# Optimization experiments

Hardware: AMD Instinct MI355X
Metric: run time of the kernel (lower is better)

Reference implementation:

```python
import jax, jax.numpy as jnp
import numpy as np


def setup_inputs() -> dict:
    key = jax.random.key(0)
    T, B, D, R = 1024, 32, 1024, 256
    ks = jax.random.split(key, 6)
    scale = 1.0 / np.sqrt(D)
    x = jax.random.normal(ks[0], (T, B, D), dtype=jnp.float32)
    h0 = jnp.zeros((B, D), dtype=jnp.float32)
    W_alpha = jax.random.normal(ks[1], (D, D), dtype=jnp.float32) * scale
    b_alpha = jnp.full((D,), 2.0, dtype=jnp.float32)  # init_alpha_bias
    U = jax.random.normal(ks[2], (D, R), dtype=jnp.float32) * (0.5 / np.sqrt(R))
    V = jax.random.normal(ks[3], (R, D), dtype=jnp.float32) * (0.5 * scale)
    W_x = jax.random.normal(ks[4], (D, D), dtype=jnp.float32) * scale
    b = jnp.zeros((D,), dtype=jnp.float32)
    return {"x": x, "h0": h0, "W_alpha": W_alpha, "b_alpha": b_alpha,
            "U": U, "V": V, "W_x": W_x, "b": b}


def reference(x, h0, W_alpha, b_alpha, U, V, W_x, b):
    # Precompute input projections for all timesteps (as in the torch fallback)
    alpha_x_all = jnp.einsum('tbd,ed->tbe', x, W_alpha) + b_alpha  # [T,B,D]
    Wx_all = jnp.einsum('tbd,ed->tbe', x, W_x) + b                 # [T,B,D]

    def step(h_prev, inp):
        ax, wx = inp
        alpha = jax.nn.sigmoid(ax)                       # retain gate
        v = jnp.tanh((h_prev @ V.T) @ U.T + wx)          # low-rank h mixing
        h_new = alpha * h_prev + (1.0 - alpha) * v
        out = h_new * jax.nn.silu(h_new)
        return h_new, (h_new, out)

    _, (h_seq, output) = jax.lax.scan(step, h0, (alpha_x_all, Wx_all))
    h = jnp.concatenate([h0[None], h_seq], axis=0)       # [T+1,B,D]
    return output, h
```

## Files before the change

### kernel.cpp

```cpp
#include <hip/hip_runtime.h>

typedef _Float16 f16;
typedef f16 f16x2 __attribute__((ext_vector_type(2)));
typedef f16 f16x8 __attribute__((ext_vector_type(8)));
typedef float f32x4 __attribute__((ext_vector_type(4)));

#define TT 1024
#define BB 32
#define DD 1024
#define RR 256

__device__ __forceinline__ float dot2f(f16x2 a, f16x2 b, float c) {
#if __has_builtin(__builtin_amdgcn_fdot2)
    return __builtin_amdgcn_fdot2(a, b, c, false);
#else
    return c + (float)a[0] * (float)b[0] + (float)a[1] * (float)b[1];
#endif
}

__device__ __forceinline__ float sigm_f(float x) { return 1.0f / (1.0f + __expf(-x)); }
__device__ __forceinline__ float tanh_f(float x) { return 1.0f - 2.0f / (1.0f + __expf(2.0f * x)); }

__global__ __launch_bounds__(256)
void fused_pregemm(const float* __restrict__ X, const float* __restrict__ Wa,
                   const float* __restrict__ Wx, const float* __restrict__ ba,
                   const float* __restrict__ bb, f16* __restrict__ axo,
                   f16* __restrict__ wxo)
{
    __shared__ __align__(16) f16 lA[64][40];
    __shared__ __align__(16) f16 lB[64][40];
    __shared__ __align__(16) f16 lC[64][40];

    const int tid = threadIdx.x;
    const int w   = tid >> 6;
    const int l   = tid & 63;
    const int la  = l & 15;
    const int qd  = l >> 4;
    const int m0  = blockIdx.x * 64;
    const int n0  = blockIdx.y * 64;
    const int sr  = tid >> 2;
    const int sk  = (tid & 3) * 8;

    f32x4 accA[4] = {};
    f32x4 accX[4] = {};

    for (int k0 = 0; k0 < DD; k0 += 32) {
        {
            const float* pX = X + (size_t)(m0 + sr) * DD + k0 + sk;
            float4 v0 = *(const float4*)pX;
            float4 v1 = *(const float4*)(pX + 4);
            f16x8 x8 = {(f16)v0.x, (f16)v0.y, (f16)v0.z, (f16)v0.w,
                        (f16)v1.x, (f16)v1.y, (f16)v1.z, (f16)v1.w};
            *(f16x8*)&lA[sr][sk] = x8;

            const float* pA = Wa + (size_t)(n0 + sr) * DD + k0 + sk;
            v0 = *(const float4*)pA;
            v1 = *(const float4*)(pA + 4);
            f16x8 a8 = {(f16)v0.x, (f16)v0.y, (f16)v0.z, (f16)v0.w,
                        (f16)v1.x, (f16)v1.y, (f16)v1.z, (f16)v1.w};
            *(f16x8*)&lB[sr][sk] = a8;

            const float* pW = Wx + (size_t)(n0 + sr) * DD + k0 + sk;
            v0 = *(const float4*)pW;
            v1 = *(const float4*)(pW + 4);
            f16x8 w8 = {(f16)v0.x, (f16)v0.y, (f16)v0.z, (f16)v0.w,
                        (f16)v1.x, (f16)v1.y, (f16)v1.z, (f16)v1.w};
            *(f16x8*)&lC[sr][sk] = w8;
        }
        __syncthreads();

        f16x8 af = *(const f16x8*)&lA[16 * w + la][qd * 8];
        #pragma unroll
        for (int c = 0; c < 4; c++) {
            f16x8 b1 = *(const f16x8*)&lB[16 * c + la][qd * 8];
            f16x8 b2 = *(const f16x8*)&lC[16 * c + la][qd * 8];
            accA[c] = __builtin_amdgcn_mfma_f32_16x16x32_f16(af, b1, accA[c], 0, 0, 0);
            accX[c] = __builtin_amdgcn_mfma_f32_16x16x32_f16(af, b2, accX[c], 0, 0, 0);
        }
        __syncthreads();
    }

    #pragma unroll
    for (int c = 0; c < 4; c++) {
        const int n = n0 + 16 * c + la;
        const float bav = ba[n];
        const float bbv = bb[n];
        #pragma unroll
        for (int r = 0; r < 4; r++) {
            const int m = m0 + 16 * w + qd * 4 + r;
            axo[(size_t)m * DD + n] = (f16)(accA[c][r] + bav);
            wxo[(size_t)m * DD + n] = (f16)(accX[c][r] + bbv);
        }
    }
}

__global__ __launch_bounds__(1024, 4)
void rnn_scan(const f16* __restrict__ ax, const f16* __restrict__ wx,
              const float* __restrict__ V, const float* __restrict__ U,
              const float* __restrict__ h0, float* __restrict__ out,
              float* __restrict__ hout)
{
    const int b   = blockIdx.x;
    const int tid = threadIdx.x;
    const int s   = tid >> 6;
    const int q   = tid & 63;
    const int e2  = tid >> 1;
    const int z   = tid & 1;

    __shared__ __align__(16) f16 h2[DD];
    __shared__ float hf[DD];
    __shared__ float part[16][RR];
    __shared__ __align__(16) f16 pl[RR];
    __shared__ float up[DD][2];

    f16x2 wv[4][32];
    #pragma unroll
    for (int j = 0; j < 4; j++) {
        const float2* vr = (const float2*)(V + (size_t)(4 * q + j) * DD + 64 * s);
        #pragma unroll
        for (int i = 0; i < 32; i++) {
            float2 t = vr[i];
            f16x2 p2 = {(f16)t.x, (f16)t.y};
            wv[j][i] = p2;
        }
    }
    f16x2 wu[2][64];
    #pragma unroll
    for (int j = 0; j < 2; j++) {
        const float2* ur = (const float2*)(U + (size_t)(2 * e2 + j) * RR + 128 * z);
        #pragma unroll
        for (int i = 0; i < 64; i++) {
            float2 t = ur[i];
            f16x2 p2 = {(f16)t.x, (f16)t.y};
            wu[j][i] = p2;
        }
    }

    const float h0v = h0[(size_t)b * DD + tid];
    hf[tid] = h0v;
    h2[tid] = (f16)h0v;
    hout[(size_t)b * DD + tid] = h0v;

    const f16* axp  = ax  + (size_t)b * DD + tid;
    const f16* wxp  = wx  + (size_t)b * DD + tid;
    float*     outp = out + (size_t)b * DD + tid;
    float*     houtp = hout + (size_t)BB * DD + (size_t)b * DD + tid;

    __syncthreads();

    #pragma unroll 1
    for (int t = 0; t < TT; t++) {
        const f16x8* hsl = (const f16x8*)(h2 + 64 * s);
        float acc[4] = {0.f, 0.f, 0.f, 0.f};
        #pragma unroll
        for (int i = 0; i < 8; i++) {
            f16x8 hv = hsl[i];
            f16x2 hp[4];
            hp[0][0] = hv[0]; hp[0][1] = hv[1];
            hp[1][0] = hv[2]; hp[1][1] = hv[3];
            hp[2][0] = hv[4]; hp[2][1] = hv[5];
            hp[3][0] = hv[6]; hp[3][1] = hv[7];
            #pragma unroll
            for (int u = 0; u < 4; u++) {
                #pragma unroll
                for (int j = 0; j < 4; j++) {
                    acc[j] = dot2f(wv[j][4 * i + u], hp[u], acc[j]);
                }
            }
        }
        part[s][4 * q + 0] = acc[0];
        part[s][4 * q + 1] = acc[1];
        part[s][4 * q + 2] = acc[2];
        part[s][4 * q + 3] = acc[3];
        __syncthreads();

        if (tid < RR) {
            float pv = 0.f;
            #pragma unroll
            for (int ss = 0; ss < 16; ss++) pv += part[ss][tid];
            pl[tid] = (f16)pv;
        }
        __syncthreads();

        const f16x8* psl = (const f16x8*)(pl + 128 * z);
        float ua[2] = {0.f, 0.f};
        #pragma unroll
        for (int i = 0; i < 16; i++) {
            f16x8 pv8 = psl[i];
            f16x2 pp[4];
            pp[0][0] = pv8[0]; pp[0][1] = pv8[1];
            pp[1][0] = pv8[2]; pp[1][1] = pv8[3];
            pp[2][0] = pv8[4]; pp[2][1] = pv8[5];
            pp[3][0] = pv8[6]; pp[3][1] = pv8[7];
            #pragma unroll
            for (int u = 0; u < 4; u++) {
                ua[0] = dot2f(wu[0][4 * i + u], pp[u], ua[0]);
                ua[1] = dot2f(wu[1][4 * i + u], pp[u], ua[1]);
            }
        }
        up[2 * e2 + 0][z] = ua[0];
        up[2 * e2 + 1][z] = ua[1];
        __syncthreads();

        {
            float uu = up[tid][0] + up[tid][1] + (float)*wxp;
            float vv = tanh_f(uu);
            float aa = sigm_f((float)*axp);
            float hp = hf[tid];
            float hn = aa * hp + (1.0f - aa) * vv;
            float so = hn * hn * sigm_f(hn);
            *outp  = so;
            *houtp = hn;
            hf[tid] = hn;
            h2[tid] = (f16)hn;
            axp += BB * DD; wxp += BB * DD; outp += BB * DD; houtp += BB * DD;
        }
        __syncthreads();
    }
}

extern "C" void kernel_launch(void* const* d_in, const int* in_sizes, int n_in,
                              void* d_out, int out_size, void* d_ws, size_t ws_size,
                              hipStream_t stream) {
    (void)in_sizes; (void)n_in; (void)out_size; (void)ws_size;
    const float* x  = (const float*)d_in[0];
    const float* h0 = (const float*)d_in[1];
    const float* Wa = (const float*)d_in[2];
    const float* ba = (const float*)d_in[3];
    const float* U  = (const float*)d_in[4];
    const float* V  = (const float*)d_in[5];
    const float* Wx = (const float*)d_in[6];
    const float* bb = (const float*)d_in[7];

    float* out  = (float*)d_out;
    float* hout = out + (size_t)TT * BB * DD;

    f16* ax16 = (f16*)d_ws;
    f16* wx16 = ax16 + (size_t)TT * BB * DD;

    dim3 g1(512, 16);
    fused_pregemm<<<g1, dim3(256), 0, stream>>>(x, Wa, Wx, ba, bb, ax16, wx16);
    rnn_scan<<<dim3(BB), dim3(1024), 0, stream>>>(ax16, wx16, V, U, h0, out, hout);
}
```

Before: 16.65 ms.

## Stream pre-packed fp16 weights from global memory and cut scan barriers

```diff
diff --git a/kernel.cpp b/kernel.cpp
--- a/kernel.cpp
+++ b/kernel.cpp
@@ -9,6 +9,9 @@
 #define BB 32
 #define DD 1024
 #define RR 256
+
+__device__ __align__(16) f16 g_VPI[RR * DD];
+__device__ __align__(16) f16 g_UPI[DD * RR];
 
 __device__ __forceinline__ float dot2f(f16x2 a, f16x2 b, float c) {
 #if __has_builtin(__builtin_amdgcn_fdot2)
@@ -94,127 +97,108 @@
     }
 }
 
+__global__ __launch_bounds__(1024)
+void pack_weights(const float* __restrict__ V, const float* __restrict__ U)
+{
+    const int i   = blockIdx.x;
+    const int tid = threadIdx.x;
+    const int r   = tid >> 2;
+    const int s2  = tid & 3;
+    const int j   = (i + s2) & 31;
+
+    const float* sv = V + (size_t)r * DD + 256 * s2 + 8 * j;
+    f16x8 v8;
+    #pragma unroll
+    for (int k = 0; k < 8; k++) v8[k] = (f16)sv[k];
+    ((f16x8*)g_VPI)[i * 1024 + tid] = v8;
+
+    const float* su = U + (size_t)tid * RR + 8 * i;
+    f16x8 u8;
+    #pragma unroll
+    for (int k = 0; k < 8; k++) u8[k] = (f16)su[k];
+    ((f16x8*)g_UPI)[i * 1024 + tid] = u8;
+}
+
 __global__ __launch_bounds__(1024, 4)
 void rnn_scan(const f16* __restrict__ ax, const f16* __restrict__ wx,
-              const float* __restrict__ V, const float* __restrict__ U,
               const float* __restrict__ h0, float* __restrict__ out,
               float* __restrict__ hout)
 {
     const int b   = blockIdx.x;
     const int tid = threadIdx.x;
-    const int s   = tid >> 6;
-    const int q   = tid & 63;
-    const int e2  = tid >> 1;
-    const int z   = tid & 1;
+    const int s2  = tid & 3;
+    const int q2  = tid >> 2;
 
     __shared__ __align__(16) f16 h2[DD];
-    __shared__ float hf[DD];
-    __shared__ float part[16][RR];
     __shared__ __align__(16) f16 pl[RR];
-    __shared__ float up[DD][2];
-
-    f16x2 wv[4][32];
-    #pragma unroll
-    for (int j = 0; j < 4; j++) {
-        const float2* vr = (const float2*)(V + (size_t)(4 * q + j) * DD + 64 * s);
-        #pragma unroll
-        for (int i = 0; i < 32; i++) {
-            float2 t = vr[i];
-            f16x2 p2 = {(f16)t.x, (f16)t.y};
-            wv[j][i] = p2;
-        }
-    }
-    f16x2 wu[2][64];
-    #pragma unroll
-    for (int j = 0; j < 2; j++) {
-        const float2* ur = (const float2*)(U + (size_t)(2 * e2 + j) * RR + 128 * z);
-        #pragma unroll
-        for (int i = 0; i < 64; i++) {
-            float2 t = ur[i];
-            f16x2 p2 = {(f16)t.x, (f16)t.y};
-            wu[j][i] = p2;
-        }
-    }
+
+    const f16x8* vp  = (const f16x8*)g_VPI + tid;
+    const f16x8* up  = (const f16x8*)g_UPI + tid;
+    const f16x8* hch = (const f16x8*)h2;
+    const f16x8* pch = (const f16x8*)pl;
 
     const float h0v = h0[(size_t)b * DD + tid];
-    hf[tid] = h0v;
+    float hreg = h0v;
     h2[tid] = (f16)h0v;
     hout[(size_t)b * DD + tid] = h0v;
 
-    const f16* axp  = ax  + (size_t)b * DD + tid;
-    const f16* wxp  = wx  + (size_t)b * DD + tid;
-    float*     outp = out + (size_t)b * DD + tid;
+    const f16* axp   = ax  + (size_t)b * DD + tid;
+    const f16* wxp   = wx  + (size_t)b * DD + tid;
+    float*     outp  = out + (size_t)b * DD + tid;
     float*     houtp = hout + (size_t)BB * DD + (size_t)b * DD + tid;
 
     __syncthreads();
 
     #pragma unroll 1
     for (int t = 0; t < TT; t++) {
-        const f16x8* hsl = (const f16x8*)(h2 + 64 * s);
-        float acc[4] = {0.f, 0.f, 0.f, 0.f};
-        #pragma unroll
-        for (int i = 0; i < 8; i++) {
-            f16x8 hv = hsl[i];
-            f16x2 hp[4];
-            hp[0][0] = hv[0]; hp[0][1] = hv[1];
-            hp[1][0] = hv[2]; hp[1][1] = hv[3];
-            hp[2][0] = hv[4]; hp[2][1] = hv[5];
-            hp[3][0] = hv[6]; hp[3][1] = hv[7];
-            #pragma unroll
-            for (int u = 0; u < 4; u++) {
-                #pragma unroll
-                for (int j = 0; j < 4; j++) {
-                    acc[j] = dot2f(wv[j][4 * i + u], hp[u], acc[j]);
-                }
-            }
-        }
-        part[s][4 * q + 0] = acc[0];
-        part[s][4 * q + 1] = acc[1];
-        part[s][4 * q + 2] = acc[2];
-        part[s][4 * q + 3] = acc[3];
-        __syncthreads();
-
-        if (tid < RR) {
-            float pv = 0.f;
-            #pragma unroll
-            for (int ss = 0; ss < 16; ss++) pv += part[ss][tid];
-            pl[tid] = (f16)pv;
-        }
-        __syncthreads();
-
-        const f16x8* psl = (const f16x8*)(pl + 128 * z);
-        float ua[2] = {0.f, 0.f};
-        #pragma unroll
-        for (int i = 0; i < 16; i++) {
-            f16x8 pv8 = psl[i];
-            f16x2 pp[4];
-            pp[0][0] = pv8[0]; pp[0][1] = pv8[1];
-            pp[1][0] = pv8[2]; pp[1][1] = pv8[3];
-            pp[2][0] = pv8[4]; pp[2][1] = pv8[5];
-            pp[3][0] = pv8[6]; pp[3][1] = pv8[7];
-            #pragma unroll
-            for (int u = 0; u < 4; u++) {
-                ua[0] = dot2f(wu[0][4 * i + u], pp[u], ua[0]);
-                ua[1] = dot2f(wu[1][4 * i + u], pp[u], ua[1]);
-            }
-        }
-        up[2 * e2 + 0][z] = ua[0];
-        up[2 * e2 + 1][z] = ua[1];
-        __syncthreads();
-
-        {
-            float uu = up[tid][0] + up[tid][1] + (float)*wxp;
-            float vv = tanh_f(uu);
-            float aa = sigm_f((float)*axp);
-            float hp = hf[tid];
-            float hn = aa * hp + (1.0f - aa) * vv;
-            float so = hn * hn * sigm_f(hn);
-            *outp  = so;
-            *houtp = hn;
-            hf[tid] = hn;
-            h2[tid] = (f16)hn;
-            axp += BB * DD; wxp += BB * DD; outp += BB * DD; houtp += BB * DD;
-        }
+        const float axv = (float)*axp;
+        const float wxv = (float)*wxp;
+
+        float a0 = 0.f, a1 = 0.f, a2 = 0.f, a3 = 0.f;
+        #pragma unroll
+        for (int i = 0; i < 32; i++) {
+            f16x8 w  = vp[(size_t)i << 10];
+            f16x8 hv = hch[32 * s2 + ((i + s2) & 31)];
+            f16x2 w0 = {w[0],  w[1]},  w1 = {w[2],  w[3]};
+            f16x2 w2 = {w[4],  w[5]},  w3 = {w[6],  w[7]};
+            f16x2 p0 = {hv[0], hv[1]}, p1 = {hv[2], hv[3]};
+            f16x2 p2 = {hv[4], hv[5]}, p3 = {hv[6], hv[7]};
+            a0 = dot2f(w0, p0, a0);
+            a1 = dot2f(w1, p1, a1);
+            a2 = dot2f(w2, p2, a2);
+            a3 = dot2f(w3, p3, a3);
+        }
+        float p = (a0 + a1) + (a2 + a3);
+        p += __shfl_xor(p, 1);
+        p += __shfl_xor(p, 2);
+        if (s2 == 0) pl[q2] = (f16)p;
+        __syncthreads();
+
+        float u0 = 0.f, u1 = 0.f, u2 = 0.f, u3 = 0.f;
+        #pragma unroll
+        for (int i = 0; i < 32; i++) {
+            f16x8 w  = up[(size_t)i << 10];
+            f16x8 pv = pch[i];
+            f16x2 w0 = {w[0],  w[1]},  w1 = {w[2],  w[3]};
+            f16x2 w2 = {w[4],  w[5]},  w3 = {w[6],  w[7]};
+            f16x2 q0 = {pv[0], pv[1]}, q1 = {pv[2], pv[3]};
+            f16x2 q2v = {pv[4], pv[5]}, q3 = {pv[6], pv[7]};
+            u0 = dot2f(w0, q0, u0);
+            u1 = dot2f(w1, q1, u1);
+            u2 = dot2f(w2, q2v, u2);
+            u3 = dot2f(w3, q3, u3);
+        }
+
+        const float uu = (u0 + u1) + (u2 + u3) + wxv;
+        const float vv = tanh_f(uu);
+        const float aa = sigm_f(axv);
+        const float hn = aa * hreg + (1.0f - aa) * vv;
+        const float so = hn * hn * sigm_f(hn);
+        *outp  = so;
+        *houtp = hn;
+        hreg = hn;
+        h2[tid] = (f16)hn;
+        axp += BB * DD; wxp += BB * DD; outp += BB * DD; houtp += BB * DD;
         __syncthreads();
     }
 }
@@ -238,7 +222,8 @@
     f16* ax16 = (f16*)d_ws;
     f16* wx16 = ax16 + (size_t)TT * BB * DD;
 
+    pack_weights<<<dim3(32), dim3(1024), 0, stream>>>(V, U);
     dim3 g1(512, 16);
     fused_pregemm<<<g1, dim3(256), 0, stream>>>(x, Wa, Wx, ba, bb, ax16, wx16);
-    rnn_scan<<<dim3(BB), dim3(1024), 0, stream>>>(ax16, wx16, V, U, h0, out, hout);
-}
+    rnn_scan<<<dim3(BB), dim3(1024), 0, stream>>>(ax16, wx16, h0, out, hout);
+}
```

Result: faster. 14.01 ms (-15.8%).
